# Kernel optimization log

Hardware: AMD Instinct MI355X
Metric: run time of the kernel (lower is better)

The kernel has to match this reference:

```python
import jax, jax.numpy as jnp
import numpy as np

B = 4096
D_IN = 1024
HIDDEN = [1024, 512, 256]
NUM_DOMAINS = 8


def _glorot(key, shape):
    fan_in, fan_out = shape[-2], shape[-1]
    std = np.sqrt(2.0 / (fan_in + fan_out)).astype(np.float32)
    return jax.random.normal(key, shape, dtype=jnp.float32) * std


def setup_inputs() -> dict:
    key = jax.random.key(0)
    keys = jax.random.split(key, 16)
    dims = [D_IN] + HIDDEN  # per-layer (in, out) = (dims[i], dims[i+1])
    inp = {
        "x": jax.random.normal(keys[0], (B, D_IN), dtype=jnp.float32),
        "indicator": jax.random.randint(keys[1], (B,), 0, NUM_DOMAINS, dtype=jnp.int32),
    }
    for i in range(len(HIDDEN)):
        inp[f"sk{i}"] = _glorot(keys[2 + i], (dims[i], dims[i + 1]))
        inp[f"sb{i}"] = jnp.zeros((dims[i + 1],), dtype=jnp.float32)
        # per-domain kernels stacked on leading domain axis: (D, in, out)
        inp[f"dk{i}"] = _glorot(keys[6 + i], (NUM_DOMAINS, dims[i], dims[i + 1]))
        inp[f"db{i}"] = jnp.zeros((NUM_DOMAINS, dims[i + 1]), dtype=jnp.float32)
    return inp


def reference(x, indicator, sk0, sb0, dk0, db0, sk1, sb1, dk1, db1, sk2, sb2, dk2, db2):
    shared_k = [sk0, sk1, sk2]
    shared_b = [sb0, sb1, sb2]
    domain_k = [dk0, dk1, dk2]
    domain_b = [db0, db1, db2]
    D = dk0.shape[0]
    # Replicate input across all domains: [B, D, d_in] (source computes every domain stack)
    h = jnp.broadcast_to(x[:, None, :], (x.shape[0], D, x.shape[1]))
    for sk, sb, dk, db in zip(shared_k, shared_b, domain_k, domain_b):
        w_eff = sk[None, :, :] * dk          # [D, in, out]  fused shared*domain weights
        b_eff = sb[None, :] + db             # [D, out]
        h = jnp.einsum('bdi,dio->bdo', h, w_eff) + b_eff[None, :, :]
        h = jax.nn.relu(h)                   # all layers use 'relu' (no output_activation)
    one_hot = jax.nn.one_hot(indicator, D, dtype=h.dtype)  # [B, D]
    return jnp.einsum('bdo,bd->bo', h, one_hot)
```

## Files before the change

### kernel.cpp

```cpp
#include <hip/hip_runtime.h>

#define NROWS 4096
#define NDOM 8

typedef short short8 __attribute__((ext_vector_type(8)));
typedef float floatx4 __attribute__((ext_vector_type(4)));
typedef unsigned short ushort8v __attribute__((ext_vector_type(8)));

__device__ __forceinline__ unsigned short f2bf(float f) {
    union { float f; unsigned u; } v; v.f = f;
    unsigned r = v.u + 0x7FFFu + ((v.u >> 16) & 1u);
    return (unsigned short)(r >> 16);
}

__device__ __forceinline__ void dma16(const void* g, void* l) {
    __builtin_amdgcn_global_load_lds(
        (const __attribute__((address_space(1))) unsigned*)g,
        (__attribute__((address_space(3))) unsigned*)l, 16, 0, 0);
}


template <int K, int N>
__device__ __forceinline__ void weff_tile(const float* __restrict__ sk,
                                          const float* __restrict__ dk,
                                          unsigned short* __restrict__ wt,
                                          unsigned short* __restrict__ lds,
                                          int local) {
    const int d = local & 7;
    const int rest = local >> 3;
    const int k0 = (rest & (K / 256 - 1)) * 256;
    const int n0 = (rest / (K / 256)) * 64;
    const int t = threadIdx.x;

    const int n = t & 63;
    const int kg = (t >> 6) * 64;
#pragma unroll
    for (int c8 = 0; c8 < 8; ++c8) {
        const int kb = k0 + kg + c8 * 8;
        unsigned short wb[8];
#pragma unroll
        for (int i = 0; i < 8; ++i) {
            int k = kb + i;
            wb[i] = f2bf(sk[(size_t)k * N + n0 + n] * dk[((size_t)d * K + k) * N + n0 + n]);
        }
        int ch = (kg + c8 * 8) >> 3;
        int phys = ch ^ (n & 31);
        *(ushort8v*)&lds[n * 256 + phys * 8] = *(ushort8v*)wb;
    }
    __syncthreads();

#pragma unroll
    for (int it = 0; it < 4; ++it) {
        const int nn = (t >> 4) + it * 16;
        const int c = t & 15;
        ushort8v a = *(ushort8v*)&lds[nn * 256 + ((2 * c) ^ (nn & 31)) * 8];
        ushort8v b = *(ushort8v*)&lds[nn * 256 + ((2 * c + 1) ^ (nn & 31)) * 8];
        unsigned short* dst = wt + ((size_t)d * N + n0 + nn) * K + k0 + c * 16;
        *(ushort8v*)dst = a;
        *(ushort8v*)(dst + 8) = b;
    }
}

__global__ void precompute_kernel(const float* __restrict__ x,
                                  const int* __restrict__ ind,
                                  const float* __restrict__ sk0, const float* __restrict__ dk0,
                                  const float* __restrict__ sk1, const float* __restrict__ dk1,
                                  const float* __restrict__ sk2, const float* __restrict__ dk2,
                                  unsigned short* __restrict__ xb,
                                  unsigned short* __restrict__ w0t,
                                  unsigned short* __restrict__ w1t,
                                  unsigned short* __restrict__ w2t,
                                  int* __restrict__ offsets,
                                  int* __restrict__ rowidx) {
    __shared__ unsigned short wtile[64 * 256];
    __shared__ unsigned short cnt[256][NDOM];
    __shared__ int base[256][NDOM];
    __shared__ int dom_total[NDOM];
    __shared__ int dom_off[NDOM + 1];

    const int b = blockIdx.x;
    const int t = threadIdx.x;

    if (b < 256) {
#pragma unroll
        for (int pass = 0; pass < 8; ++pass) {
            int row = b * 16 + pass * 2 + (t >> 7);
            int ch = t & 127;
            const float* src = x + (size_t)row * 1024 + ch * 8;
            floatx4 v0 = *(const floatx4*)src;
            floatx4 v1 = *(const floatx4*)(src + 4);
            unsigned short o[8];
            o[0] = f2bf(v0[0]); o[1] = f2bf(v0[1]); o[2] = f2bf(v0[2]); o[3] = f2bf(v0[3]);
            o[4] = f2bf(v1[0]); o[5] = f2bf(v1[1]); o[6] = f2bf(v1[2]); o[7] = f2bf(v1[3]);
            *(ushort8v*)(xb + (size_t)row * 1024 + ch * 8) = *(ushort8v*)o;
        }
    } else if (b < 256 + 512) {
        weff_tile<1024, 1024>(sk0, dk0, w0t, wtile, b - 256);
    } else if (b < 256 + 512 + 256) {
        weff_tile<1024, 512>(sk1, dk1, w1t, wtile, b - (256 + 512));
    } else if (b < 256 + 512 + 256 + 64) {
        weff_tile<512, 256>(sk2, dk2, w2t, wtile, b - (256 + 512 + 256));
    } else {
        int myind[16];
#pragma unroll
        for (int i = 0; i < 16; ++i) myind[i] = ind[t * 16 + i];
        unsigned short c[NDOM];
#pragma unroll
        for (int d = 0; d < NDOM; ++d) c[d] = 0;
#pragma unroll
        for (int i = 0; i < 16; ++i) c[myind[i]]++;
#pragma unroll
        for (int d = 0; d < NDOM; ++d) cnt[t][d] = c[d];
        __syncthreads();
        if (t < NDOM) {
            int acc = 0;
            for (int ch = 0; ch < 256; ++ch) { base[ch][t] = acc; acc += cnt[ch][t]; }
            dom_total[t] = acc;
        }
        __syncthreads();
        if (t == 0) {
            int acc = 0;
            for (int d = 0; d < NDOM; ++d) { dom_off[d] = acc; acc += dom_total[d]; }
            dom_off[NDOM] = acc;
        }
        __syncthreads();
        int pos[NDOM];
#pragma unroll
        for (int d = 0; d < NDOM; ++d) pos[d] = dom_off[d] + base[t][d];
#pragma unroll
        for (int i = 0; i < 16; ++i) {
            int dm = myind[i];
            rowidx[pos[dm]++] = t * 16 + i;
        }
        if (t <= NDOM) offsets[t] = dom_off[t];
    }
}

template <int FM, int FN, int MSLOTS, int K, int N, bool GATHER, bool SCATTER>
__launch_bounds__(256)
__global__ void star_gemm(const unsigned short* __restrict__ Ab,
                          const unsigned short* __restrict__ Wt,
                          const float* __restrict__ sb,
                          const float* __restrict__ db,
                          float* __restrict__ OutF,
                          unsigned short* __restrict__ OutB,
                          const int* __restrict__ offsets,
                          const int* __restrict__ rowidx) {
    constexpr int BM = 32 * FM;
    constexpr int BN = 32 * FN;
    constexpr int NK = K / 64;
    constexpr int AI = BM / 32;
    constexpr int WI = BN / 32;

    __shared__ __align__(128) unsigned short As[2][BM * 64];
    __shared__ __align__(128) unsigned short Ws[2][BN * 64];

    const int gid = blockIdx.x;
    const int d = gid & 7;
    const int mslot = (gid >> 3) % MSLOTS;
    const int n0 = (gid / (8 * MSLOTS)) * BN;

    const int bstart = offsets[d];
    const int bend = offsets[d + 1];
    const int bsize = bend - bstart;

    const int tid = threadIdx.x;
    const int lane = tid & 63;
    const int w = tid >> 6;
    const int wy = w >> 1;
    const int wx = w & 1;
    const int lm = lane & 15;
    const int quad = lane >> 4;

    const int lrow = lane >> 3;
    const int phys = lane & 7;

    float bias[FN];
#pragma unroll
    for (int j = 0; j < FN; ++j) {
        int n = n0 + wx * FN * 16 + j * 16 + lm;
        bias[j] = sb[n] + db[d * N + n];
    }

    const unsigned short* wsrc[WI];
#pragma unroll
    for (int j = 0; j < WI; ++j) {
        int nr0 = (w * WI + j) * 8;
        int nn = nr0 + lrow;
        int ch = phys ^ (nn & 7);
        wsrc[j] = Wt + ((size_t)d * N + n0 + nn) * K + ch * 8;
    }

    for (int mt = mslot; mt * BM < bsize; mt += MSLOTS) {
        const int row_start = bstart + mt * BM;

        const unsigned short* asrc[AI];
#pragma unroll
        for (int j = 0; j < AI; ++j) {
            int m0 = (w * AI + j) * 8;
            int mm = m0 + lrow;
            int ch = phys ^ (mm & 7);
            int p = row_start + mm; if (p >= bend) p = bend - 1;
            int src = GATHER ? rowidx[p] : p;
            asrc[j] = Ab + (size_t)src * K + ch * 8;
        }

        auto dma_tiles = [&](int kt, int buf) {
            const int k0 = kt * 64;
#pragma unroll
            for (int j = 0; j < AI; ++j)
                dma16(asrc[j] + k0, &As[buf][(w * AI + j) * 512]);
#pragma unroll
            for (int j = 0; j < WI; ++j)
                dma16(wsrc[j] + k0, &Ws[buf][(w * WI + j) * 512]);
        };

        floatx4 acc[FM][FN];
#pragma unroll
        for (int i = 0; i < FM; ++i)
#pragma unroll
            for (int j = 0; j < FN; ++j) acc[i][j] = floatx4{0.f, 0.f, 0.f, 0.f};

        dma_tiles(0, 0);
        for (int kt = 0; kt < NK; ++kt) {
            const int buf = kt & 1;
            __syncthreads();

            short8 av[2][FM], wv[2][FN];
#pragma unroll
            for (int kk = 0; kk < 2; ++kk) {
#pragma unroll
                for (int i = 0; i < FM; ++i) {
                    int m = wy * FM * 16 + i * 16 + lm;
                    int pc = (kk * 4 + quad) ^ (m & 7);
                    av[kk][i] = *(const short8*)&As[buf][m * 64 + pc * 8];
                }
#pragma unroll
                for (int j = 0; j < FN; ++j) {
                    int n = wx * FN * 16 + j * 16 + lm;
                    int pc = (kk * 4 + quad) ^ (n & 7);
                    wv[kk][j] = *(const short8*)&Ws[buf][n * 64 + pc * 8];
                }
            }
            if (kt + 1 < NK) dma_tiles(kt + 1, 1 - buf);
#pragma unroll
            for (int kk = 0; kk < 2; ++kk)
#pragma unroll
                for (int i = 0; i < FM; ++i)
#pragma unroll
                    for (int j = 0; j < FN; ++j)
                        acc[i][j] = __builtin_amdgcn_mfma_f32_16x16x32_bf16(
                            av[kk][i], wv[kk][j], acc[i][j], 0, 0, 0);
        }

#pragma unroll
        for (int i = 0; i < FM; ++i) {
#pragma unroll
            for (int rg = 0; rg < 4; ++rg) {
                int m = wy * FM * 16 + i * 16 + quad * 4 + rg;
                int p = row_start + m;
                if (p < bend) {
                    if constexpr (SCATTER) {
                        int orow = rowidx[p];
#pragma unroll
                        for (int j = 0; j < FN; ++j) {
                            int n = n0 + wx * FN * 16 + j * 16 + lm;
                            float v = acc[i][j][rg] + bias[j];
                            OutF[(size_t)orow * N + n] = v > 0.f ? v : 0.f;
                        }
                    } else {
#pragma unroll
                        for (int j = 0; j < FN; ++j) {
                            int n = n0 + wx * FN * 16 + j * 16 + lm;
                            float v = acc[i][j][rg] + bias[j];
                            OutB[(size_t)p * N + n] = f2bf(v > 0.f ? v : 0.f);
                        }
                    }
                }
            }
        }
    }
}

extern "C" void kernel_launch(void* const* d_in, const int* in_sizes, int n_in,
                              void* d_out, int out_size, void* d_ws, size_t ws_size,
                              hipStream_t stream) {
    const float* x = (const float*)d_in[0];
    const int* ind = (const int*)d_in[1];
    const float* sk0 = (const float*)d_in[2];
    const float* sb0 = (const float*)d_in[3];
    const float* dk0 = (const float*)d_in[4];
    const float* db0 = (const float*)d_in[5];
    const float* sk1 = (const float*)d_in[6];
    const float* sb1 = (const float*)d_in[7];
    const float* dk1 = (const float*)d_in[8];
    const float* db1 = (const float*)d_in[9];
    const float* sk2 = (const float*)d_in[10];
    const float* sb2 = (const float*)d_in[11];
    const float* dk2 = (const float*)d_in[12];
    const float* db2 = (const float*)d_in[13];
    float* out = (float*)d_out;

    char* ws = (char*)d_ws;
    int* offsets = (int*)ws;
    int* rowidx = (int*)(ws + 256);
    unsigned short* xb  = (unsigned short*)(ws + 32768);
    unsigned short* h1  = xb + (size_t)NROWS * 1024;
    unsigned short* h2  = h1 + (size_t)NROWS * 1024;
    unsigned short* w0t = h2 + (size_t)NROWS * 512;
    unsigned short* w1t = w0t + (size_t)NDOM * 1024 * 1024;
    unsigned short* w2t = w1t + (size_t)NDOM * 512 * 1024;

    precompute_kernel<<<256 + 512 + 256 + 64 + 1, 256, 0, stream>>>(
        x, ind, sk0, dk0, sk1, dk1, sk2, dk2, xb, w0t, w1t, w2t, offsets, rowidx);

    star_gemm<2, 2, 8, 1024, 1024, true, false><<<1024, 256, 0, stream>>>(
        xb, w0t, sb0, db0, nullptr, h1, offsets, rowidx);
    star_gemm<2, 2, 8, 1024, 512, false, false><<<512, 256, 0, stream>>>(
        h1, w1t, sb1, db1, nullptr, h2, offsets, rowidx);
    star_gemm<1, 2, 16, 512, 256, false, true><<<512, 256, 0, stream>>>(
        h2, w2t, sb2, db2, out, nullptr, offsets, rowidx);
}
```

Before: 187.4 us.

## Issue next-tile DMA before compute with explicit vmcnt waits and split barriers

Restructures the GEMM main loop so the next K-tile's global-to-LDS DMA is issued at the top of each iteration, followed by a partial vmcnt wait that leaves only the newest loads in flight. A second barrier after the LDS reads makes the double buffer safe, and s_setprio raises wave priority around the MFMA block. The loop is unrolled by 2. The goal is to overlap memory latency with compute more deterministically than the compiler-inserted waits did, at the cost of an extra barrier per iteration. The precompute kernel's shared arrays are also put into a union to cut LDS footprint.

```diff
diff --git a/kernel.cpp b/kernel.cpp
--- a/kernel.cpp
+++ b/kernel.cpp
@@ -17,6 +17,17 @@
     __builtin_amdgcn_global_load_lds(
         (const __attribute__((address_space(1))) unsigned*)g,
         (__attribute__((address_space(3))) unsigned*)l, 16, 0, 0);
+}
+
+template <int N>
+__device__ __forceinline__ void wait_vmcnt() {
+    static_assert(N == 0 || N == 2 || N == 3 || N == 4 || N == 6 || N == 8, "unsupported vmcnt");
+    if constexpr (N == 0) asm volatile("s_waitcnt vmcnt(0)" ::: "memory");
+    else if constexpr (N == 2) asm volatile("s_waitcnt vmcnt(2)" ::: "memory");
+    else if constexpr (N == 3) asm volatile("s_waitcnt vmcnt(3)" ::: "memory");
+    else if constexpr (N == 4) asm volatile("s_waitcnt vmcnt(4)" ::: "memory");
+    else if constexpr (N == 6) asm volatile("s_waitcnt vmcnt(6)" ::: "memory");
+    else if constexpr (N == 8) asm volatile("s_waitcnt vmcnt(8)" ::: "memory");
 }
 
 
@@ -72,11 +83,15 @@
                                   unsigned short* __restrict__ w2t,
                                   int* __restrict__ offsets,
                                   int* __restrict__ rowidx) {
-    __shared__ unsigned short wtile[64 * 256];
-    __shared__ unsigned short cnt[256][NDOM];
-    __shared__ int base[256][NDOM];
-    __shared__ int dom_total[NDOM];
-    __shared__ int dom_off[NDOM + 1];
+    __shared__ union SMem {
+        unsigned short wtile[64 * 256];
+        struct {
+            unsigned short cnt[256][NDOM];
+            int base[256][NDOM];
+            int dom_total[NDOM];
+            int dom_off[NDOM + 1];
+        } sort;
+    } smem;
 
     const int b = blockIdx.x;
     const int t = threadIdx.x;
@@ -95,11 +110,11 @@
             *(ushort8v*)(xb + (size_t)row * 1024 + ch * 8) = *(ushort8v*)o;
         }
     } else if (b < 256 + 512) {
-        weff_tile<1024, 1024>(sk0, dk0, w0t, wtile, b - 256);
+        weff_tile<1024, 1024>(sk0, dk0, w0t, smem.wtile, b - 256);
     } else if (b < 256 + 512 + 256) {
-        weff_tile<1024, 512>(sk1, dk1, w1t, wtile, b - (256 + 512));
+        weff_tile<1024, 512>(sk1, dk1, w1t, smem.wtile, b - (256 + 512));
     } else if (b < 256 + 512 + 256 + 64) {
-        weff_tile<512, 256>(sk2, dk2, w2t, wtile, b - (256 + 512 + 256));
+        weff_tile<512, 256>(sk2, dk2, w2t, smem.wtile, b - (256 + 512 + 256));
     } else {
         int myind[16];
 #pragma unroll
@@ -110,29 +125,29 @@
 #pragma unroll
         for (int i = 0; i < 16; ++i) c[myind[i]]++;
 #pragma unroll
-        for (int d = 0; d < NDOM; ++d) cnt[t][d] = c[d];
+        for (int d = 0; d < NDOM; ++d) smem.sort.cnt[t][d] = c[d];
         __syncthreads();
         if (t < NDOM) {
             int acc = 0;
-            for (int ch = 0; ch < 256; ++ch) { base[ch][t] = acc; acc += cnt[ch][t]; }
-            dom_total[t] = acc;
+            for (int ch = 0; ch < 256; ++ch) { smem.sort.base[ch][t] = acc; acc += smem.sort.cnt[ch][t]; }
+            smem.sort.dom_total[t] = acc;
         }
         __syncthreads();
         if (t == 0) {
             int acc = 0;
-            for (int d = 0; d < NDOM; ++d) { dom_off[d] = acc; acc += dom_total[d]; }
-            dom_off[NDOM] = acc;
+            for (int d = 0; d < NDOM; ++d) { smem.sort.dom_off[d] = acc; acc += smem.sort.dom_total[d]; }
+            smem.sort.dom_off[NDOM] = acc;
         }
         __syncthreads();
         int pos[NDOM];
 #pragma unroll
-        for (int d = 0; d < NDOM; ++d) pos[d] = dom_off[d] + base[t][d];
+        for (int d = 0; d < NDOM; ++d) pos[d] = smem.sort.dom_off[d] + smem.sort.base[t][d];
 #pragma unroll
         for (int i = 0; i < 16; ++i) {
             int dm = myind[i];
             rowidx[pos[dm]++] = t * 16 + i;
         }
-        if (t <= NDOM) offsets[t] = dom_off[t];
+        if (t <= NDOM) offsets[t] = smem.sort.dom_off[t];
     }
 }
 
@@ -151,6 +166,7 @@
     constexpr int NK = K / 64;
     constexpr int AI = BM / 32;
     constexpr int WI = BN / 32;
+    constexpr int CNT = AI + WI;
 
     __shared__ __align__(128) unsigned short As[2][BM * 64];
     __shared__ __align__(128) unsigned short Ws[2][BN * 64];
@@ -215,16 +231,25 @@
                 dma16(wsrc[j] + k0, &Ws[buf][(w * WI + j) * 512]);
         };
 
+        dma_tiles(0, 0);
+
         floatx4 acc[FM][FN];
 #pragma unroll
         for (int i = 0; i < FM; ++i)
 #pragma unroll
             for (int j = 0; j < FN; ++j) acc[i][j] = floatx4{0.f, 0.f, 0.f, 0.f};
 
-        dma_tiles(0, 0);
+#pragma unroll 2
         for (int kt = 0; kt < NK; ++kt) {
             const int buf = kt & 1;
-            __syncthreads();
+            if (kt + 1 < NK) {
+                dma_tiles(kt + 1, 1 - buf);
+                wait_vmcnt<CNT>();
+            } else {
+                wait_vmcnt<0>();
+            }
+            __builtin_amdgcn_s_barrier();
+            asm volatile("" ::: "memory");
 
             short8 av[2][FM], wv[2][FN];
 #pragma unroll
@@ -242,7 +267,12 @@
                     wv[kk][j] = *(const short8*)&Ws[buf][n * 64 + pc * 8];
                 }
             }
-            if (kt + 1 < NK) dma_tiles(kt + 1, 1 - buf);
+            asm volatile("s_waitcnt lgkmcnt(0)" ::: "memory");
+            __builtin_amdgcn_sched_barrier(0);
+            __builtin_amdgcn_s_barrier();
+            asm volatile("" ::: "memory");
+
+            __builtin_amdgcn_s_setprio(1);
 #pragma unroll
             for (int kk = 0; kk < 2; ++kk)
 #pragma unroll
@@ -251,6 +281,7 @@
                     for (int j = 0; j < FN; ++j)
                         acc[i][j] = __builtin_amdgcn_mfma_f32_16x16x32_bf16(
                             av[kk][i], wv[kk][j], acc[i][j], 0, 0, 0);
+            __builtin_amdgcn_s_setprio(0);
         }
 
 #pragma unroll
```

Result: slower. 191.2 us (+2.0%).
